# Kernel tuning notes

Measured on AMD Instinct MI355X. Metric: run time of the kernel, lower is better.

The kernel has to match this reference:

```python
import jax, jax.numpy as jnp
import numpy as np

B, S, HID = 2, 1024, 2048
NH, NKV, HD = 16, 4, 128
SCALE = 1.0 / np.sqrt(HD)
ROPE_BASE = 10000.0
EPS = 1e-6


def setup_inputs() -> dict:
    key = jax.random.key(0)
    ks = jax.random.split(key, 5)
    std = 0.02
    return {
        "hidden_states": jax.random.normal(ks[0], (B, S, HID), jnp.float32),
        "Wq": jax.random.normal(ks[1], (NH * HD, HID), jnp.float32) * std,
        "Wk": jax.random.normal(ks[2], (NKV * HD, HID), jnp.float32) * std,
        "Wv": jax.random.normal(ks[3], (NKV * HD, HID), jnp.float32) * std,
        "Wo": jax.random.normal(ks[4], (HID, HID), jnp.float32) * std,
        "q_norm_w": jnp.ones((HD,), jnp.float32),
        "k_norm_w": jnp.ones((HD,), jnp.float32),
    }


def _rope(x):
    # x: [B, H, S, D]; half-split rotary
    d2 = HD // 2
    inv_freq = 1.0 / (ROPE_BASE ** (jnp.arange(0, HD, 2, dtype=jnp.float32) / HD))
    ang = jnp.arange(S, dtype=jnp.float32)[:, None] * inv_freq[None, :]  # [S, d2]
    cos, sin = jnp.cos(ang), jnp.sin(ang)
    x1, x2 = x[..., :d2], x[..., d2:]
    return jnp.concatenate([x1 * cos - x2 * sin, x1 * sin + x2 * cos], axis=-1)


def _rms(x, w):
    var = jnp.mean(jnp.square(x), axis=-1, keepdims=True)
    return x * jax.lax.rsqrt(var + EPS) * w


def reference(hidden_states, Wq, Wk, Wv, Wo, q_norm_w, k_norm_w):
    b, s, _ = hidden_states.shape
    # projections (no bias)
    q = (hidden_states @ Wq.T).reshape(b, s, NH, HD).transpose(0, 2, 1, 3)
    k = (hidden_states @ Wk.T).reshape(b, s, NKV, HD).transpose(0, 2, 1, 3)
    v = (hidden_states @ Wv.T).reshape(b, s, NKV, HD).transpose(0, 2, 1, 3)
    # RoPE then per-head-dim RMS qk-norm (shared params across heads)
    q, k = _rope(q), _rope(k)
    q, k = _rms(q, q_norm_w), _rms(k, k_norm_w)
    # GQA: repeat kv heads
    groups = NH // NKV
    k = jnp.repeat(k, groups, axis=1)
    v = jnp.repeat(v, groups, axis=1)
    # stick-breaking attention, strictly causal (attend_current=False), no normalize
    logits = jnp.einsum("bhid,bhjd->bhij", q, k) * SCALE  # [B,H,S,S]
    log_p = jax.nn.log_sigmoid(logits)
    log_om = jax.nn.log_sigmoid(-logits)  # log(1 - p)
    i = jnp.arange(s)
    mask = i[None, :] < i[:, None]  # j < i
    masked_om = jnp.where(mask, log_om, 0.0)
    # cum[i,j] = sum_{j < k < i} log(1-p[i,k]) : exclusive reversed cumsum
    cum = jnp.flip(jnp.cumsum(jnp.flip(masked_om, -1), -1), -1) - masked_om
    att = jnp.where(mask, jnp.exp(log_p + cum), 0.0)
    o = jnp.einsum("bhij,bhjd->bhid", att, v)
    o = o.transpose(0, 2, 1, 3).reshape(b, s, NH * HD)
    return o @ Wo.T
```

## Files before the change

### kernel.cpp

```cpp
#include <hip/hip_runtime.h>
#include <math.h>

#define B_    2
#define S_    1024
#define HID_  2048
#define NH_   16
#define NKV_  4
#define HD_   128
#define GROUPS (NH_ / NKV_)
#define SCALE_ 0.08838834764831845f

typedef _Float16 f16x8 __attribute__((ext_vector_type(8)));
typedef float    f32x4 __attribute__((ext_vector_type(4)));

__device__ __forceinline__ void async_copy16(const void* g, void* l) {
    __builtin_amdgcn_global_load_lds(
        (const __attribute__((address_space(1))) void*)g,
        (__attribute__((address_space(3))) void*)l, 16, 0, 0);
}

__device__ __forceinline__ int dpp_swap1(int x) {
    return __builtin_amdgcn_update_dpp(0, x, 0xB1, 0xF, 0xF, true);
}

__global__ __launch_bounds__(256) void cast4_f16(
    const float4* __restrict__ s0, ushort4* __restrict__ d0, int n0,
    const float4* __restrict__ s1, ushort4* __restrict__ d1, int n1,
    const float4* __restrict__ s2, ushort4* __restrict__ d2, int n2,
    const float4* __restrict__ s3, ushort4* __restrict__ d3, int n3)
{
    int i = blockIdx.x * 256 + threadIdx.x;
    const float4* s; ushort4* d; int idx;
    if (i < n0)                { s = s0; d = d0; idx = i; }
    else if (i < n0 + n1)      { s = s1; d = d1; idx = i - n0; }
    else if (i < n0 + n1 + n2) { s = s2; d = d2; idx = i - n0 - n1; }
    else if (i < n0 + n1 + n2 + n3) { s = s3; d = d3; idx = i - n0 - n1 - n2; }
    else return;
    float4 v = s[idx];
    _Float16 a = (_Float16)v.x, b = (_Float16)v.y,
             c = (_Float16)v.z, e = (_Float16)v.w;
    ushort4 o;
    o.x = *(unsigned short*)&a; o.y = *(unsigned short*)&b;
    o.z = *(unsigned short*)&c; o.w = *(unsigned short*)&e;
    d[idx] = o;
}

__global__ __launch_bounds__(256) void cast_f16(
    const float4* __restrict__ x, ushort4* __restrict__ y, int n4)
{
    int i = blockIdx.x * 256 + threadIdx.x;
    if (i >= n4) return;
    float4 v = x[i];
    _Float16 a = (_Float16)v.x, b = (_Float16)v.y,
             c = (_Float16)v.z, e = (_Float16)v.w;
    ushort4 o;
    o.x = *(unsigned short*)&a; o.y = *(unsigned short*)&b;
    o.z = *(unsigned short*)&c; o.w = *(unsigned short*)&e;
    y[i] = o;
}

__global__ __launch_bounds__(256) void qkv_gemm(
    const _Float16* __restrict__ A,
    const _Float16* __restrict__ Wq,
    const _Float16* __restrict__ Wk,
    const _Float16* __restrict__ Wv,
    _Float16* __restrict__ Cq, _Float16* __restrict__ Ck,
    _Float16* __restrict__ Cv)
{
    __shared__ __align__(16) _Float16 As[128][32];
    __shared__ __align__(16) _Float16 Ws[128][32];

    const int tid  = threadIdx.x;
    const int lane = tid & 63, wave = tid >> 6;
    const int wr = (wave >> 1) * 64, wc = (wave & 1) * 64;
    const int bm = blockIdx.y * 128;
    const int bt = blockIdx.x;

    const _Float16* Wsel;
    _Float16* Csel;
    int nrow0, heads;
    if (bt < 16)      { Wsel = Wq; Csel = Cq; nrow0 = bt * 128;        heads = NH_;  }
    else if (bt < 20) { Wsel = Wk; Csel = Ck; nrow0 = (bt - 16) * 128; heads = NKV_; }
    else              { Wsel = Wv; Csel = Cv; nrow0 = (bt - 20) * 128; heads = NKV_; }

    const int srow = 32 * wave + (lane >> 2);
    const int scol = (lane & 3) * 8;
    const _Float16* Ag = A    + (size_t)(bm + srow)    * HID_ + scol;
    const _Float16* Wg = Wsel + (size_t)(nrow0 + srow) * HID_ + scol;
    _Float16* lA = &As[32 * wave][0];
    _Float16* lW = &Ws[32 * wave][0];

    f32x4 acc[4][4];
    const f32x4 fz = {0.f, 0.f, 0.f, 0.f};
#pragma unroll
    for (int i = 0; i < 4; i++)
#pragma unroll
        for (int j = 0; j < 4; j++) acc[i][j] = fz;

    const int ml = lane & 15, kg = lane >> 4;

    for (int k0 = 0; k0 < HID_; k0 += 32) {
        __syncthreads();
        async_copy16(Ag + k0, lA);
        async_copy16(Ag + k0 + (size_t)16 * HID_, lA + 16 * 32);
        async_copy16(Wg + k0, lW);
        async_copy16(Wg + k0 + (size_t)16 * HID_, lW + 16 * 32);
        __syncthreads();

        f16x8 a[4], b[4];
#pragma unroll
        for (int mi = 0; mi < 4; mi++)
            a[mi] = *(const f16x8*)&As[wr + mi * 16 + ml][kg * 8];
#pragma unroll
        for (int ni = 0; ni < 4; ni++)
            b[ni] = *(const f16x8*)&Ws[wc + ni * 16 + ml][kg * 8];
#pragma unroll
        for (int mi = 0; mi < 4; mi++)
#pragma unroll
            for (int ni = 0; ni < 4; ni++)
                acc[mi][ni] = __builtin_amdgcn_mfma_f32_16x16x32_f16(
                    a[mi], b[ni], acc[mi][ni], 0, 0, 0);
    }

#pragma unroll
    for (int mi = 0; mi < 4; mi++) {
#pragma unroll
        for (int ni = 0; ni < 4; ni++) {
#pragma unroll
            for (int r = 0; r < 4; r++) {
                int m = bm + wr + mi * 16 + kg * 4 + r;
                int n = nrow0 + wc + ni * 16 + ml;
                int hh = n >> 7, d = n & 127;
                int b_ = m >> 10, s = m & 1023;
                size_t idx = (((size_t)(b_ * heads + hh)) * S_ + s) * HD_ + d;
                Csel[idx] = (_Float16)acc[mi][ni][r];
            }
        }
    }
}

__global__ __launch_bounds__(256) void out_gemm(
    const _Float16* __restrict__ A,
    const _Float16* __restrict__ W,
    float* __restrict__ C)
{
    __shared__ __align__(16) _Float16 As[128][32];
    __shared__ __align__(16) _Float16 Ws[128][32];

    const int tid  = threadIdx.x;
    const int lane = tid & 63, wave = tid >> 6;
    const int wr = (wave >> 1) * 64, wc = (wave & 1) * 64;
    const int bm = blockIdx.y * 128, bn = blockIdx.x * 128;

    const int srow = 32 * wave + (lane >> 2);
    const int scol = (lane & 3) * 8;
    const _Float16* Ag = A + (size_t)(bm + srow) * HID_ + scol;
    const _Float16* Wg = W + (size_t)(bn + srow) * HID_ + scol;
    _Float16* lA = &As[32 * wave][0];
    _Float16* lW = &Ws[32 * wave][0];

    f32x4 acc[4][4];
    const f32x4 fz = {0.f, 0.f, 0.f, 0.f};
#pragma unroll
    for (int i = 0; i < 4; i++)
#pragma unroll
        for (int j = 0; j < 4; j++) acc[i][j] = fz;

    const int ml = lane & 15, kg = lane >> 4;

    for (int k0 = 0; k0 < HID_; k0 += 32) {
        __syncthreads();
        async_copy16(Ag + k0, lA);
        async_copy16(Ag + k0 + (size_t)16 * HID_, lA + 16 * 32);
        async_copy16(Wg + k0, lW);
        async_copy16(Wg + k0 + (size_t)16 * HID_, lW + 16 * 32);
        __syncthreads();

        f16x8 a[4], b[4];
#pragma unroll
        for (int mi = 0; mi < 4; mi++)
            a[mi] = *(const f16x8*)&As[wr + mi * 16 + ml][kg * 8];
#pragma unroll
        for (int ni = 0; ni < 4; ni++)
            b[ni] = *(const f16x8*)&Ws[wc + ni * 16 + ml][kg * 8];
#pragma unroll
        for (int mi = 0; mi < 4; mi++)
#pragma unroll
            for (int ni = 0; ni < 4; ni++)
                acc[mi][ni] = __builtin_amdgcn_mfma_f32_16x16x32_f16(
                    a[mi], b[ni], acc[mi][ni], 0, 0, 0);
    }

#pragma unroll
    for (int mi = 0; mi < 4; mi++)
#pragma unroll
        for (int ni = 0; ni < 4; ni++)
#pragma unroll
            for (int r = 0; r < 4; r++) {
                int m = bm + wr + mi * 16 + kg * 4 + r;
                int n = bn + wc + ni * 16 + ml;
                C[(size_t)m * HID_ + n] = acc[mi][ni][r];
            }
}

__global__ __launch_bounds__(256) void rope_rms_f16(
    const _Float16* __restrict__ Qin, const _Float16* __restrict__ Kin,
    const float* __restrict__ qw, const float* __restrict__ kw,
    _Float16* __restrict__ Qout, _Float16* __restrict__ Kout)
{
    int row = blockIdx.x * 4 + (threadIdx.x >> 6);
    int lane = threadIdx.x & 63;
    bool isQ = row < 32768;
    int lrow = isQ ? row : row - 32768;
    const _Float16* p = (isQ ? Qin : Kin) + (size_t)lrow * HD_;
    _Float16* q = (isQ ? Qout : Kout) + (size_t)lrow * HD_;
    const float* w = isQ ? qw : kw;
    int s = row & (S_ - 1);

    float x1 = (float)p[lane], x2 = (float)p[lane + 64];

    float invf = exp2f(-(float)lane * 0.2076205059304601f);
    float ang = (float)s * invf;
    float c, sn;
    sincosf(ang, &sn, &c);

    float y1 = x1 * c - x2 * sn;
    float y2 = x1 * sn + x2 * c;

    float ss = y1 * y1 + y2 * y2;
#pragma unroll
    for (int off = 32; off > 0; off >>= 1) ss += __shfl_xor(ss, off);

    float scl = rsqrtf(ss * (1.0f / 128.0f) + 1e-6f);
    q[lane]      = (_Float16)(y1 * scl * w[lane]);
    q[lane + 64] = (_Float16)(y2 * scl * w[lane + 64]);
}

#define QK_STR 136
#define VT_STR 72
#define SS_STR 68
#define AT_STR 72

__global__ __launch_bounds__(512) void stick_attn(
    const _Float16* __restrict__ Q, const _Float16* __restrict__ K,
    const _Float16* __restrict__ V, _Float16* __restrict__ AO)
{
    __shared__ __align__(16) _Float16 Qs[64][QK_STR];
    __shared__ __align__(16) _Float16 Ks[64][QK_STR];
    __shared__ __align__(16) _Float16 Vt[128][VT_STR];
    __shared__ __align__(16) float    Ss[64][SS_STR];
    __shared__ __align__(16) _Float16 atts[64][AT_STR];
    __shared__ float paccs[64];

    const int bid = blockIdx.x;
    const int slot = bid & 255, phase = bid >> 8;
    const int hb = slot >> 3, iw = slot & 7;
    const int b = hb >> 4, h = hb & 15;
    const int qb = phase ? iw : 15 - iw;

    const int kvh = h / GROUPS;
    const int tid = threadIdx.x;
    const int lane = tid & 63, wave = tid >> 6;
    const int qw = wave >> 1;
    const int kh = wave & 1;
    const int ml = lane & 15, quad = lane >> 4;

    const _Float16* Kbase = K + ((size_t)(b * NKV_ + kvh) * S_) * HD_;
    const _Float16* Vbase = V + ((size_t)(b * NKV_ + kvh) * S_) * HD_;

    const f32x4 fz = {0.f, 0.f, 0.f, 0.f};

    const int qi0 = qb * 64;
    const _Float16* Qbase = Q + ((size_t)(b * NH_ + h) * S_ + qi0) * HD_;

    for (int idx = tid; idx < 64 * 16; idx += 512) {
        int r = idx >> 4, c8 = (idx & 15) * 8;
        *(f16x8*)&Qs[r][c8] = *(const f16x8*)(Qbase + r * HD_ + c8);
    }
    if (tid < 64) paccs[tid] = 1.f;
    __syncthreads();

    f16x8 aq[4];
#pragma unroll
    for (int ks = 0; ks < 4; ks++)
        aq[ks] = *(const f16x8*)&Qs[qw * 16 + ml][ks * 32 + quad * 8];

    f32x4 accO[4] = {fz, fz, fz, fz};

    for (int kb = qb; kb >= 0; --kb) {
        __syncthreads();

        for (int idx = tid; idx < 64 * 16; idx += 512) {
            int r = idx >> 4, c8 = (idx & 15) * 8;
            *(f16x8*)&Ks[r][c8] =
                *(const f16x8*)(Kbase + (size_t)(kb * 64 + r) * HD_ + c8);
        }
        {
            int key = lane, dg = wave;
            const _Float16* vp =
                Vbase + (size_t)(kb * 64 + key) * HD_ + dg * 16;
            f16x8 v0 = *(const f16x8*)(vp);
            f16x8 v1 = *(const f16x8*)(vp + 8);
            int4 i0 = *(int4*)&v0, i1 = *(int4*)&v1;
            int4 p0, p1;
            p0.x = dpp_swap1(i0.x); p0.y = dpp_swap1(i0.y);
            p0.z = dpp_swap1(i0.z); p0.w = dpp_swap1(i0.w);
            p1.x = dpp_swap1(i1.x); p1.y = dpp_swap1(i1.y);
            p1.z = dpp_swap1(i1.z); p1.w = dpp_swap1(i1.w);
            bool ev = !(lane & 1);
            int4 al = ev ? i0 : p1;
            int4 bh = ev ? p0 : i1;
            int r0w = dg * 16 + (ev ? 0 : 8);
            int colk = lane & ~1;
            int ac[4] = {al.x, al.y, al.z, al.w};
            int bc[4] = {bh.x, bh.y, bh.z, bh.w};
#pragma unroll
            for (int i = 0; i < 8; i++) {
                int c = i >> 1;
                unsigned pack = (i & 1)
                    ? (((unsigned)ac[c] >> 16) | ((unsigned)bc[c] & 0xffff0000u))
                    : (((unsigned)ac[c] & 0xffffu) | ((unsigned)bc[c] << 16));
                *(unsigned*)&Vt[r0w + i][colk] = pack;
            }
        }
        __syncthreads();

        f32x4 accS[2] = {fz, fz};
#pragma unroll
        for (int ks = 0; ks < 4; ks++) {
#pragma unroll
            for (int ni = 0; ni < 2; ni++) {
                f16x8 bf = *(const f16x8*)
                    &Ks[kh * 32 + ni * 16 + ml][ks * 32 + quad * 8];
                accS[ni] = __builtin_amdgcn_mfma_f32_16x16x32_f16(
                    aq[ks], bf, accS[ni], 0, 0, 0);
            }
        }
#pragma unroll
        for (int ni = 0; ni < 2; ni++)
#pragma unroll
            for (int r = 0; r < 4; r++)
                Ss[qw * 16 + quad * 4 + r][kh * 32 + ni * 16 + ml] =
                    accS[ni][r] * SCALE_;
        __syncthreads();

        {
            int q = tid >> 3, seg = tid & 7;
            int qg = qi0 + q;
            int j0 = kb * 64 + seg * 8;
            float4 s0 = *(float4*)&Ss[q][seg * 8];
            float4 s1 = *(float4*)&Ss[q][seg * 8 + 4];
            float L[8] = {s0.x, s0.y, s0.z, s0.w, s1.x, s1.y, s1.z, s1.w};
            float sv[8], om[8];
#pragma unroll
            for (int i = 0; i < 8; i++) {
                float u = __expf(L[i]);
                float o = __builtin_amdgcn_rcpf(1.f + u);
                bool valid = (j0 + i < qg);
                om[i] = valid ? o : 1.f;
                sv[i] = valid ? (1.f - o) : 0.f;
            }
            float suf = 1.f, lo[8];
#pragma unroll
            for (int i = 7; i >= 0; --i) {
                lo[i] = suf; suf *= om[i];
            }
            float x = suf;
#pragma unroll
            for (int off = 1; off < 8; off <<= 1) {
                float y = __shfl_down(x, off);
                if (seg + off < 8) x *= y;
            }
            float bx = __shfl_down(x, 1);
            float base = (seg == 7) ? 1.f : bx;
            float paccq = paccs[q];
            float pb = base * paccq;
            f16x8 av;
#pragma unroll
            for (int i = 0; i < 8; i++)
                av[i] = (_Float16)(sv[i] * lo[i] * pb);
            *(f16x8*)&atts[q][seg * 8] = av;
            if (seg == 0) paccs[q] = paccq * x;
        }
        __syncthreads();

#pragma unroll
        for (int ks = 0; ks < 2; ks++) {
            f16x8 ap = *(const f16x8*)&atts[qw * 16 + ml][ks * 32 + quad * 8];
#pragma unroll
            for (int ni = 0; ni < 4; ni++) {
                f16x8 bv = *(const f16x8*)
                    &Vt[kh * 64 + ni * 16 + ml][ks * 32 + quad * 8];
                accO[ni] = __builtin_amdgcn_mfma_f32_16x16x32_f16(
                    ap, bv, accO[ni], 0, 0, 0);
            }
        }
    }

#pragma unroll
    for (int ni = 0; ni < 4; ni++) {
#pragma unroll
        for (int r = 0; r < 4; r++) {
            int qg = qi0 + qw * 16 + quad * 4 + r;
            int d = kh * 64 + ni * 16 + ml;
            AO[((size_t)(b * S_ + qg) * NH_ + h) * HD_ + d] =
                (_Float16)accO[ni][r];
        }
    }
}

extern "C" void kernel_launch(void* const* d_in, const int* in_sizes, int n_in,
                              void* d_out, int out_size, void* d_ws, size_t ws_size,
                              hipStream_t stream)
{
    const float* hs = (const float*)d_in[0];
    const float* Wq = (const float*)d_in[1];
    const float* Wk = (const float*)d_in[2];
    const float* Wv = (const float*)d_in[3];
    const float* Wo = (const float*)d_in[4];
    const float* qw = (const float*)d_in[5];
    const float* kw = (const float*)d_in[6];
    float* out = (float*)d_out;

    _Float16* Qg  = (_Float16*)d_ws;
    _Float16* Kg  = Qg + 4194304;
    _Float16* pad = Kg + 1048576;
    _Float16* hsh = (_Float16*)((float*)d_ws + 5242880);
    _Float16* Wqh = hsh + 4194304;
    _Float16* Wkh = Wqh + 4194304;
    _Float16* Wvh = Wkh + 1048576;
    _Float16* Qh  = Wvh + 1048576;
    _Float16* Kh  = Qh + 4194304;
    _Float16* Vh  = Kh + 1048576;
    _Float16* AOh = hsh;
    _Float16* Woh = Wqh;
    (void)pad;

    dim3 blk(256);

    cast4_f16<<<10240, blk, 0, stream>>>(
        (const float4*)hs, (ushort4*)hsh, 1048576,
        (const float4*)Wq, (ushort4*)Wqh, 1048576,
        (const float4*)Wk, (ushort4*)Wkh, 262144,
        (const float4*)Wv, (ushort4*)Wvh, 262144);

    qkv_gemm<<<dim3(24, 16), blk, 0, stream>>>(hsh, Wqh, Wkh, Wvh,
                                               Qg, Kg, Vh);

    cast_f16<<<4096, blk, 0, stream>>>((const float4*)Wo, (ushort4*)Woh, 1048576);

    rope_rms_f16<<<dim3((32768 + 8192) / 4), blk, 0, stream>>>(
        Qg, Kg, qw, kw, Qh, Kh);

    stick_attn<<<dim3(512), dim3(512), 0, stream>>>(Qh, Kh, Vh, AOh);

    out_gemm<<<dim3(16, 16), blk, 0, stream>>>(AOh, Woh, out);
}
```

Baseline: 248.7 us.

## Split-K both projection GEMMs with fp32 atomic accumulation

```diff
diff --git a/kernel.cpp b/kernel.cpp
--- a/kernel.cpp
+++ b/kernel.cpp
@@ -23,18 +23,20 @@
     return __builtin_amdgcn_update_dpp(0, x, 0xB1, 0xF, 0xF, true);
 }
 
-__global__ __launch_bounds__(256) void cast4_f16(
+__global__ __launch_bounds__(256) void cast5_f16(
     const float4* __restrict__ s0, ushort4* __restrict__ d0, int n0,
     const float4* __restrict__ s1, ushort4* __restrict__ d1, int n1,
     const float4* __restrict__ s2, ushort4* __restrict__ d2, int n2,
-    const float4* __restrict__ s3, ushort4* __restrict__ d3, int n3)
+    const float4* __restrict__ s3, ushort4* __restrict__ d3, int n3,
+    const float4* __restrict__ s4, ushort4* __restrict__ d4, int n4)
 {
     int i = blockIdx.x * 256 + threadIdx.x;
     const float4* s; ushort4* d; int idx;
-    if (i < n0)                { s = s0; d = d0; idx = i; }
-    else if (i < n0 + n1)      { s = s1; d = d1; idx = i - n0; }
-    else if (i < n0 + n1 + n2) { s = s2; d = d2; idx = i - n0 - n1; }
-    else if (i < n0 + n1 + n2 + n3) { s = s3; d = d3; idx = i - n0 - n1 - n2; }
+    if (i < n0)                          { s = s0; d = d0; idx = i; }
+    else if (i < n0 + n1)                { s = s1; d = d1; idx = i - n0; }
+    else if (i < n0 + n1 + n2)           { s = s2; d = d2; idx = i - n0 - n1; }
+    else if (i < n0 + n1 + n2 + n3)      { s = s3; d = d3; idx = i - n0 - n1 - n2; }
+    else if (i < n0 + n1 + n2 + n3 + n4) { s = s4; d = d4; idx = i - n0 - n1 - n2 - n3; }
     else return;
     float4 v = s[idx];
     _Float16 a = (_Float16)v.x, b = (_Float16)v.y,
@@ -45,27 +47,12 @@
     d[idx] = o;
 }
 
-__global__ __launch_bounds__(256) void cast_f16(
-    const float4* __restrict__ x, ushort4* __restrict__ y, int n4)
-{
-    int i = blockIdx.x * 256 + threadIdx.x;
-    if (i >= n4) return;
-    float4 v = x[i];
-    _Float16 a = (_Float16)v.x, b = (_Float16)v.y,
-             c = (_Float16)v.z, e = (_Float16)v.w;
-    ushort4 o;
-    o.x = *(unsigned short*)&a; o.y = *(unsigned short*)&b;
-    o.z = *(unsigned short*)&c; o.w = *(unsigned short*)&e;
-    y[i] = o;
-}
-
 __global__ __launch_bounds__(256) void qkv_gemm(
     const _Float16* __restrict__ A,
     const _Float16* __restrict__ Wq,
     const _Float16* __restrict__ Wk,
     const _Float16* __restrict__ Wv,
-    _Float16* __restrict__ Cq, _Float16* __restrict__ Ck,
-    _Float16* __restrict__ Cv)
+    float* __restrict__ Cq, float* __restrict__ Ck, float* __restrict__ Cv)
 {
     __shared__ __align__(16) _Float16 As[128][32];
     __shared__ __align__(16) _Float16 Ws[128][32];
@@ -75,9 +62,10 @@
     const int wr = (wave >> 1) * 64, wc = (wave & 1) * 64;
     const int bm = blockIdx.y * 128;
     const int bt = blockIdx.x;
+    const int kbase = blockIdx.z * (HID_ / 2);
 
     const _Float16* Wsel;
-    _Float16* Csel;
+    float* Csel;
     int nrow0, heads;
     if (bt < 16)      { Wsel = Wq; Csel = Cq; nrow0 = bt * 128;        heads = NH_;  }
     else if (bt < 20) { Wsel = Wk; Csel = Ck; nrow0 = (bt - 16) * 128; heads = NKV_; }
@@ -85,8 +73,8 @@
 
     const int srow = 32 * wave + (lane >> 2);
     const int scol = (lane & 3) * 8;
-    const _Float16* Ag = A    + (size_t)(bm + srow)    * HID_ + scol;
-    const _Float16* Wg = Wsel + (size_t)(nrow0 + srow) * HID_ + scol;
+    const _Float16* Ag = A    + (size_t)(bm + srow)    * HID_ + kbase + scol;
+    const _Float16* Wg = Wsel + (size_t)(nrow0 + srow) * HID_ + kbase + scol;
     _Float16* lA = &As[32 * wave][0];
     _Float16* lW = &Ws[32 * wave][0];
 
@@ -99,7 +87,7 @@
 
     const int ml = lane & 15, kg = lane >> 4;
 
-    for (int k0 = 0; k0 < HID_; k0 += 32) {
+    for (int k0 = 0; k0 < HID_ / 2; k0 += 32) {
         __syncthreads();
         async_copy16(Ag + k0, lA);
         async_copy16(Ag + k0 + (size_t)16 * HID_, lA + 16 * 32);
@@ -133,7 +121,7 @@
                 int hh = n >> 7, d = n & 127;
                 int b_ = m >> 10, s = m & 1023;
                 size_t idx = (((size_t)(b_ * heads + hh)) * S_ + s) * HD_ + d;
-                Csel[idx] = (_Float16)acc[mi][ni][r];
+                atomicAdd(&Csel[idx], acc[mi][ni][r]);
             }
         }
     }
@@ -151,11 +139,12 @@
     const int lane = tid & 63, wave = tid >> 6;
     const int wr = (wave >> 1) * 64, wc = (wave & 1) * 64;
     const int bm = blockIdx.y * 128, bn = blockIdx.x * 128;
+    const int kbase = blockIdx.z * (HID_ / 2);
 
     const int srow = 32 * wave + (lane >> 2);
     const int scol = (lane & 3) * 8;
-    const _Float16* Ag = A + (size_t)(bm + srow) * HID_ + scol;
-    const _Float16* Wg = W + (size_t)(bn + srow) * HID_ + scol;
+    const _Float16* Ag = A + (size_t)(bm + srow) * HID_ + kbase + scol;
+    const _Float16* Wg = W + (size_t)(bn + srow) * HID_ + kbase + scol;
     _Float16* lA = &As[32 * wave][0];
     _Float16* lW = &Ws[32 * wave][0];
 
@@ -168,7 +157,7 @@
 
     const int ml = lane & 15, kg = lane >> 4;
 
-    for (int k0 = 0; k0 < HID_; k0 += 32) {
+    for (int k0 = 0; k0 < HID_ / 2; k0 += 32) {
         __syncthreads();
         async_copy16(Ag + k0, lA);
         async_copy16(Ag + k0 + (size_t)16 * HID_, lA + 16 * 32);
@@ -199,25 +188,38 @@
             for (int r = 0; r < 4; r++) {
                 int m = bm + wr + mi * 16 + kg * 4 + r;
                 int n = bn + wc + ni * 16 + ml;
-                C[(size_t)m * HID_ + n] = acc[mi][ni][r];
-            }
-}
-
-__global__ __launch_bounds__(256) void rope_rms_f16(
-    const _Float16* __restrict__ Qin, const _Float16* __restrict__ Kin,
+                atomicAdd(&C[(size_t)m * HID_ + n], acc[mi][ni][r]);
+            }
+}
+
+__global__ __launch_bounds__(256) void rope_rms_v(
+    const float* __restrict__ Qin, const float* __restrict__ Kin,
+    const float* __restrict__ Vin,
     const float* __restrict__ qw, const float* __restrict__ kw,
-    _Float16* __restrict__ Qout, _Float16* __restrict__ Kout)
+    _Float16* __restrict__ Qout, _Float16* __restrict__ Kout,
+    _Float16* __restrict__ Vout)
 {
     int row = blockIdx.x * 4 + (threadIdx.x >> 6);
     int lane = threadIdx.x & 63;
+
+    if (row >= 40960) {
+        int lrow = row - 40960;
+        const float* p = Vin + (size_t)lrow * HD_;
+        _Float16* q = Vout + (size_t)lrow * HD_;
+        float2 v0 = *(const float2*)(p + lane * 2);
+        q[lane * 2]     = (_Float16)v0.x;
+        q[lane * 2 + 1] = (_Float16)v0.y;
+        return;
+    }
+
     bool isQ = row < 32768;
     int lrow = isQ ? row : row - 32768;
-    const _Float16* p = (isQ ? Qin : Kin) + (size_t)lrow * HD_;
+    const float* p = (isQ ? Qin : Kin) + (size_t)lrow * HD_;
     _Float16* q = (isQ ? Qout : Kout) + (size_t)lrow * HD_;
     const float* w = isQ ? qw : kw;
     int s = row & (S_ - 1);
 
-    float x1 = (float)p[lane], x2 = (float)p[lane + 64];
+    float x1 = p[lane], x2 = p[lane + 64];
 
     float invf = exp2f(-(float)lane * 0.2076205059304601f);
     float ang = (float)s * invf;
@@ -422,37 +424,38 @@
     const float* kw = (const float*)d_in[6];
     float* out = (float*)d_out;
 
-    _Float16* Qg  = (_Float16*)d_ws;
-    _Float16* Kg  = Qg + 4194304;
-    _Float16* pad = Kg + 1048576;
-    _Float16* hsh = (_Float16*)((float*)d_ws + 5242880);
+    float* q32 = (float*)d_ws;
+    float* k32 = q32 + 4194304;
+    float* v32 = k32 + 1048576;
+    _Float16* hsh = (_Float16*)(v32 + 1048576);
     _Float16* Wqh = hsh + 4194304;
     _Float16* Wkh = Wqh + 4194304;
     _Float16* Wvh = Wkh + 1048576;
-    _Float16* Qh  = Wvh + 1048576;
+    _Float16* Woh = Wvh + 1048576;
+    _Float16* Qh  = Woh + 4194304;
     _Float16* Kh  = Qh + 4194304;
     _Float16* Vh  = Kh + 1048576;
     _Float16* AOh = hsh;
-    _Float16* Woh = Wqh;
-    (void)pad;
 
     dim3 blk(256);
 
-    cast4_f16<<<10240, blk, 0, stream>>>(
+    cast5_f16<<<14336, blk, 0, stream>>>(
         (const float4*)hs, (ushort4*)hsh, 1048576,
         (const float4*)Wq, (ushort4*)Wqh, 1048576,
         (const float4*)Wk, (ushort4*)Wkh, 262144,
-        (const float4*)Wv, (ushort4*)Wvh, 262144);
-
-    qkv_gemm<<<dim3(24, 16), blk, 0, stream>>>(hsh, Wqh, Wkh, Wvh,
-                                               Qg, Kg, Vh);
-
-    cast_f16<<<4096, blk, 0, stream>>>((const float4*)Wo, (ushort4*)Woh, 1048576);
-
-    rope_rms_f16<<<dim3((32768 + 8192) / 4), blk, 0, stream>>>(
-        Qg, Kg, qw, kw, Qh, Kh);
+        (const float4*)Wv, (ushort4*)Wvh, 262144,
+        (const float4*)Wo, (ushort4*)Woh, 1048576);
+
+    hipMemsetAsync(q32, 0, (size_t)(4194304 + 1048576 + 1048576) * 4, stream);
+    hipMemsetAsync(out, 0, (size_t)4194304 * 4, stream);
+
+    qkv_gemm<<<dim3(24, 16, 2), blk, 0, stream>>>(hsh, Wqh, Wkh, Wvh,
+                                                  q32, k32, v32);
+
+    rope_rms_v<<<dim3(49152 / 4), blk, 0, stream>>>(
+        q32, k32, v32, qw, kw, Qh, Kh, Vh);
 
     stick_attn<<<dim3(512), dim3(512), 0, stream>>>(Qh, Kh, Vh, AOh);
 
-    out_gemm<<<dim3(16, 16), blk, 0, stream>>>(AOh, Woh, out);
-}
+    out_gemm<<<dim3(16, 16, 2), blk, 0, stream>>>(AOh, Woh, out);
+}
```

Measured after the change: 297.3 us. 19.5% more time.
